# Kernel optimization log

Hardware: AMD Instinct MI355X
Metric: run time of the kernel (lower is better)

Reference implementation:

```python
import jax, jax.numpy as jnp
import numpy as np

B, S, D, V, H, L, NM = 16, 512, 768, 30522, 12, 12, 77
HD = D // H  # 64
FF = 4 * D
EPS = 1e-5


def setup_inputs() -> dict:
    key = jax.random.key(0)
    ks = jax.random.split(key, 32)
    sc = 0.02
    n = lambda k, shp: jax.random.normal(k, shp, dtype=jnp.float32) * sc
    d = {}
    d["token_ids"] = jax.random.randint(ks[0], (B, S), 0, V)
    d["segment_ids"] = jax.random.randint(ks[1], (B, S), 0, 2)
    d["mask_ids"] = jax.random.randint(ks[2], (B, NM), 0, S)
    d["tok_emb"] = n(ks[3], (V, D))
    d["pos_emb"] = n(ks[4], (S, D))
    d["seg_emb"] = n(ks[5], (2, D))
    d["dense_w"] = n(ks[6], (V, D))
    d["dense_b"] = jnp.zeros((V,), jnp.float32)
    # per-layer params stacked on leading L axis (torch Linear convention: y = x @ W.T + b)
    d["Wq"] = n(ks[7], (L, D, D)); d["bq"] = jnp.zeros((L, D), jnp.float32)
    d["Wk"] = n(ks[8], (L, D, D)); d["bk"] = jnp.zeros((L, D), jnp.float32)
    d["Wv"] = n(ks[9], (L, D, D)); d["bv"] = jnp.zeros((L, D), jnp.float32)
    d["Wo"] = n(ks[10], (L, D, D)); d["bo"] = jnp.zeros((L, D), jnp.float32)
    d["W1"] = n(ks[11], (L, FF, D)); d["b1"] = jnp.zeros((L, FF), jnp.float32)
    d["W2"] = n(ks[12], (L, D, FF)); d["b2"] = jnp.zeros((L, D), jnp.float32)
    d["g1"] = jnp.ones((L, D), jnp.float32); d["be1"] = jnp.zeros((L, D), jnp.float32)
    d["g2"] = jnp.ones((L, D), jnp.float32); d["be2"] = jnp.zeros((L, D), jnp.float32)
    return d


def _ln(x, g, b):
    m = jnp.mean(x, -1, keepdims=True)
    v = jnp.mean(jnp.square(x - m), -1, keepdims=True)
    return (x - m) * jax.lax.rsqrt(v + EPS) * g + b


def _encoder_stack(x, layer_params):
    def layer(x, p):
        Wq, bq, Wk, bk, Wv, bv, Wo, bo, W1, b1, W2, b2, g1, be1, g2, be2 = p
        q = (x @ Wq.T + bq).reshape(B, S, H, HD).transpose(0, 2, 1, 3)  # bhsd
        k = (x @ Wk.T + bk).reshape(B, S, H, HD).transpose(0, 2, 1, 3)
        v = (x @ Wv.T + bv).reshape(B, S, H, HD).transpose(0, 2, 1, 3)
        scores = jnp.einsum('bhqd,bhkd->bhqk', q, k) / jnp.sqrt(jnp.float32(HD))
        attn = jax.nn.softmax(scores, axis=-1)
        o = jnp.einsum('bhqk,bhkd->bhqd', attn, v).transpose(0, 2, 1, 3).reshape(B, S, D)
        x = _ln(x + (o @ Wo.T + bo), g1, be1)
        h = jax.nn.gelu(x @ W1.T + b1, approximate=False)  # torch nn.GELU default is exact
        h = h @ W2.T + b2
        return _ln(x + h, g2, be2), None
    x, _ = jax.lax.scan(layer, x, layer_params)
    return x


def reference(token_ids, segment_ids, mask_ids, tok_emb, pos_emb, seg_emb,
              dense_w, dense_b, Wq, bq, Wk, bk, Wv, bv, Wo, bo,
              W1, b1, W2, b2, g1, be1, g2, be2):
    x = tok_emb[token_ids] + seg_emb[segment_ids] + pos_emb[None, :, :]  # [B,S,D]
    x = _encoder_stack(x, (Wq, bq, Wk, bk, Wv, bv, Wo, bo, W1, b1, W2, b2, g1, be1, g2, be2))
    idx = jnp.broadcast_to(mask_ids[:, :, None], (B, NM, D))
    out = jnp.take_along_axis(x, idx, axis=1)  # [B,NM,D]
    return out @ dense_w.T + dense_b  # [B,NM,V]
```

## Files before the change

kernel.cpp:

```cpp
#include <hip/hip_runtime.h>
#include <stdint.h>

typedef uint16_t u16;
typedef uint32_t u32;
typedef uint64_t u64;
typedef short short8 __attribute__((ext_vector_type(8)));
typedef float f32x4 __attribute__((ext_vector_type(4)));

#define DEV static __device__ __forceinline__

DEV u16 f2bf(float f){
  u32 x = __builtin_bit_cast(u32, f);
  return (u16)((x + 0x7fffu + ((x >> 16) & 1u)) >> 16);
}

DEV f32x4 mfma16(short8 a, short8 b, f32x4 c){
  return __builtin_amdgcn_mfma_f32_16x16x32_bf16(a, b, c, 0, 0, 0);
}

DEV void async16(const void* g, void* l){
  __builtin_amdgcn_global_load_lds(
      (const __attribute__((address_space(1))) u32*)g,
      (__attribute__((address_space(3))) u32*)l, 16, 0, 0);
}

__global__ __launch_bounds__(256)
void embed_kernel(const int* __restrict__ tid, const int* __restrict__ sid,
                  const float* __restrict__ tok, const float* __restrict__ pos,
                  const float* __restrict__ seg,
                  float* __restrict__ x, u16* __restrict__ xb)
{
  const int row = blockIdx.x;
  const int s = row & 511;
  const int tk = tid[row], sg = sid[row];
  const int t = threadIdx.x;
#pragma unroll
  for (int e = 0; e < 3; ++e){
    int i = t + e*256;
    float v = tok[(u64)tk*768 + i] + seg[(u64)sg*768 + i] + pos[(u64)s*768 + i];
    x[(u64)row*768 + i] = v;
    xb[(u64)row*768 + i] = f2bf(v);
  }
}

__global__ __launch_bounds__(256)
void cvt_bf16(const float4* __restrict__ in, ushort4* __restrict__ out, int n4)
{
  int i = blockIdx.x*256 + threadIdx.x;
  if (i >= n4) return;
  float4 f = in[i];
  ushort4 o;
  o.x = f2bf(f.x); o.y = f2bf(f.y); o.z = f2bf(f.z); o.w = f2bf(f.w);
  out[i] = o;
}

__global__ __launch_bounds__(256)
void cvt_layer(const float4* __restrict__ Wq, const float4* __restrict__ Wk,
               const float4* __restrict__ Wv, const float4* __restrict__ Wo,
               const float4* __restrict__ W1, const float4* __restrict__ W2,
               ushort4* __restrict__ wqkv, ushort4* __restrict__ wob,
               ushort4* __restrict__ w1b, ushort4* __restrict__ w2b)
{
  const int i = blockIdx.x*256 + threadIdx.x;
  const int S = 147456;
  float4 f; ushort4* dst; int di;
  if      (i <   S)       { f = Wq[i];            dst = wqkv; di = i; }
  else if (i < 2*S)       { f = Wk[i - S];        dst = wqkv; di = i; }
  else if (i < 3*S)       { f = Wv[i - 2*S];      dst = wqkv; di = i; }
  else if (i < 4*S)       { f = Wo[i - 3*S];      dst = wob;  di = i - 3*S; }
  else if (i < 4*S+589824){ f = W1[i - 4*S];      dst = w1b;  di = i - 4*S; }
  else                    { f = W2[i - 4*S-589824]; dst = w2b; di = i - 4*S - 589824; }
  ushort4 o;
  o.x = f2bf(f.x); o.y = f2bf(f.y); o.z = f2bf(f.z); o.w = f2bf(f.w);
  dst[di] = o;
}

__global__ __launch_bounds__(256)
void concat_bias(const float* __restrict__ bq, const float* __restrict__ bk,
                 const float* __restrict__ bv, float* __restrict__ out)
{
  const int l = blockIdx.x;
  const int t = threadIdx.x;
#pragma unroll
  for (int e = 0; e < 3; ++e){
    int i = t + e*256;
    out[(u64)l*2304 + i]        = bq[(u64)l*768 + i];
    out[(u64)l*2304 + 768 + i]  = bk[(u64)l*768 + i];
    out[(u64)l*2304 + 1536 + i] = bv[(u64)l*768 + i];
  }
}

template<int EPI>
__global__ __launch_bounds__(256)
void gemm_db(const u16* __restrict__ A, const u16* __restrict__ W,
             const float* __restrict__ bias, void* __restrict__ Cout,
             int M, int N, int K, int GM)
{
  __shared__ u16 smbuf[16384];
  u16* As = smbuf;
  u16* Ws = smbuf + 8192;
  const int t = threadIdx.x;
  const int w = t >> 6, l = t & 63;
  const int lr = l & 15, lg = l >> 4;

  const int nwg = gridDim.x;
  const int orig = blockIdx.x;
  const int q = nwg >> 3, r = nwg & 7;
  const int xcd = orig & 7, slot = orig >> 3;
  const int wgid = (xcd < r ? xcd*(q+1) : r*(q+1) + (xcd-r)*q) + slot;
  const int bm = wgid % GM, bn = wgid / GM;

  const u16* srcp[4];
  u16* ldsp[4];
#pragma unroll
  for (int i = 0; i < 4; ++i){
    int c = w*4 + i;
    int rt = (c & 7)*16 + (l >> 2);
    int col = (l & 3)*8;
    if (c < 8){
      int row = bm*128 + rt; if (row > M-1) row = M-1;
      srcp[i] = A + (u64)row*K + col;
      ldsp[i] = &As[c*512 + l*8];
    } else {
      int row = bn*128 + rt; if (row > N-1) row = N-1;
      srcp[i] = W + (u64)row*K + col;
      ldsp[i] = &Ws[(c - 8)*512 + l*8];
    }
  }

  const int wm = (w >> 1)*64, wn = (w & 1)*64;
  f32x4 acc[4][4] = {};

  const int nt = K >> 5;
  int buf = 0;
#pragma unroll
  for (int i = 0; i < 4; ++i) async16(srcp[i], ldsp[i]);
  __syncthreads();

  for (int kt = 0; kt < nt; ++kt){
    if (kt + 1 < nt){
      const int k0 = (kt + 1) << 5;
#pragma unroll
      for (int i = 0; i < 4; ++i) async16(srcp[i] + k0, ldsp[i] + (buf ^ 1)*4096);
    }
    short8 af[4], wf[4];
#pragma unroll
    for (int mi = 0; mi < 4; ++mi)
      af[mi] = *(const short8*)(&As[buf*4096 + (wm + mi*16 + lr)*32 + lg*8]);
#pragma unroll
    for (int ni = 0; ni < 4; ++ni)
      wf[ni] = *(const short8*)(&Ws[buf*4096 + (wn + ni*16 + lr)*32 + lg*8]);
#pragma unroll
    for (int mi = 0; mi < 4; ++mi)
#pragma unroll
      for (int ni = 0; ni < 4; ++ni)
        acc[mi][ni] = mfma16(af[mi], wf[ni], acc[mi][ni]);
    if (kt + 1 < nt){
      __syncthreads();
      buf ^= 1;
    }
  }

  __syncthreads();
  constexpr int EPLD = 68;
  float* epw = (float*)smbuf + w*(16*EPLD);
#pragma unroll
  for (int mi = 0; mi < 4; ++mi){
#pragma unroll
    for (int ni = 0; ni < 4; ++ni){
      int col = bn*128 + wn + ni*16 + lr;
      float bv = bias ? bias[col < N ? col : N-1] : 0.f;
#pragma unroll
      for (int rr = 0; rr < 4; ++rr){
        float v = acc[mi][ni][rr] + bv;
        if constexpr (EPI == 2) v = 0.5f*v*(1.0f + erff(v*0.70710678118f));
        epw[(lg*4 + rr)*EPLD + ni*16 + lr] = v;
      }
    }
    asm volatile("s_waitcnt lgkmcnt(0)" ::: "memory");
    if constexpr (EPI == 0){
#pragma unroll
      for (int ps = 0; ps < 4; ++ps){
        int rloc = ps*4 + (l >> 4);
        int row = bm*128 + wm + mi*16 + rloc;
        int col = bn*128 + wn + (l & 15)*4;
        f32x4 v4 = *(const f32x4*)&epw[rloc*EPLD + (l & 15)*4];
        if (row < M){
          if (col + 3 < N) *(f32x4*)((float*)Cout + (u64)row*N + col) = v4;
          else {
#pragma unroll
            for (int j = 0; j < 4; ++j)
              if (col + j < N) ((float*)Cout)[(u64)row*N + col + j] = v4[j];
          }
        }
      }
    } else {
#pragma unroll
      for (int ps = 0; ps < 2; ++ps){
        int rloc = ps*8 + (l >> 3);
        int row = bm*128 + wm + mi*16 + rloc;
        int col = bn*128 + wn + (l & 7)*8;
        f32x4 a4 = *(const f32x4*)&epw[rloc*EPLD + (l & 7)*8];
        f32x4 b4 = *(const f32x4*)&epw[rloc*EPLD + (l & 7)*8 + 4];
        short8 o8;
        o8[0] = f2bf(a4[0]); o8[1] = f2bf(a4[1]); o8[2] = f2bf(a4[2]); o8[3] = f2bf(a4[3]);
        o8[4] = f2bf(b4[0]); o8[5] = f2bf(b4[1]); o8[6] = f2bf(b4[2]); o8[7] = f2bf(b4[3]);
        if (row < M){
          if (col + 7 < N) *(short8*)((u16*)Cout + (u64)row*N + col) = o8;
          else {
#pragma unroll
            for (int j = 0; j < 8; ++j)
              if (col + j < N) ((u16*)Cout)[(u64)row*N + col + j] = (u16)o8[j];
          }
        }
      }
    }
    asm volatile("s_waitcnt lgkmcnt(0)" ::: "memory");
  }
}

DEV void stage_tile(const u16* __restrict__ X, int ld, int limit,
                    int rowbase, int k0, u16* lds, int t)
{
  const int rl  = t >> 2;
  const int col = (((t & 3) ^ ((t >> 3) & 3))) << 3;
  int r0 = rowbase + rl;        if (r0 > limit-1) r0 = limit-1;
  int r1 = rowbase + rl + 128;  if (r1 > limit-1) r1 = limit-1;
  async16(X + (u64)r0*ld + k0 + col, lds + t*8);
  async16(X + (u64)r1*ld + k0 + col, lds + 4096 + t*8);
}

DEV short8 ldfrag(const u16* buf, int row, int slot){
  return *(const short8*)(buf + row*32 + (slot << 3));
}

template<int EPI>
__global__ __launch_bounds__(512)
void gemm8(const u16* __restrict__ A, const u16* __restrict__ W,
           const float* __restrict__ bias, void* __restrict__ Cout,
           int M, int N, int Ksp, int lda, int ldw, int GM, int nsplit,
           u64 cstride)
{
  __shared__ u16 sm[49152];
  u16* Ab = sm;
  u16* Bb = sm + 24576;
  const int t = threadIdx.x;
  const int w = t >> 6, l = t & 63;
  const int lr = l & 15, lg = l >> 4;
  const int wr = w >> 2, wc = w & 3;
  const int xr = (lr >> 1) & 3;
  const int slot = lg ^ xr;

  const int nwg = gridDim.x, orig = blockIdx.x;
  const int q = nwg >> 3, r = nwg & 7;
  const int xcd = orig & 7, sl8 = orig >> 3;
  const int wgid = (xcd < r ? xcd*(q+1) : r*(q+1) + (xcd-r)*q) + sl8;
  const int per = nwg / nsplit;
  const int split = wgid / per;
  const int rem = wgid % per;
  const int bm = rem % GM, bn = rem / GM;
  const int koff = split * Ksp;

  f32x4 acc[8][4] = {};
  short8 afr[4], bfr[4];

  const int NT = Ksp >> 5;
  stage_tile(A, lda, M, bm*256, koff,      Ab,        t);
  stage_tile(W, ldw, N, bn*256, koff,      Bb,        t);
  if (NT > 1){
    stage_tile(A, lda, M, bm*256, koff + 32, Ab + 8192, t);
    stage_tile(W, ldw, N, bn*256, koff + 32, Bb + 8192, t);
  }
  asm volatile("s_waitcnt vmcnt(4)" ::: "memory");
  __builtin_amdgcn_s_barrier();

  for (int tt = 0; tt < NT; ++tt){
    const int rs = (tt % 3) * 8192;
    const int rs2 = ((tt + 2) % 3) * 8192;
    const int k2 = koff + (tt + 2)*32;
    const u16* Ar = Ab + rs;
    const u16* Br = Bb + rs;
#pragma unroll
    for (int mi = 0; mi < 4; ++mi) afr[mi] = ldfrag(Ar, wr*128 + mi*16 + lr, slot);
#pragma unroll
    for (int ni = 0; ni < 4; ++ni) bfr[ni] = ldfrag(Br, wc*64 + ni*16 + lr, slot);
    if (tt + 2 < NT) stage_tile(A, lda, M, bm*256, k2, Ab + rs2, t);
    __builtin_amdgcn_s_barrier();
    __builtin_amdgcn_s_setprio(1);
#pragma unroll
    for (int mi = 0; mi < 4; ++mi)
#pragma unroll
      for (int ni = 0; ni < 4; ++ni)
        acc[mi][ni] = mfma16(afr[mi], bfr[ni], acc[mi][ni]);
    __builtin_amdgcn_s_setprio(0);
    __builtin_amdgcn_s_barrier();
#pragma unroll
    for (int mi = 0; mi < 4; ++mi) afr[mi] = ldfrag(Ar, wr*128 + (mi+4)*16 + lr, slot);
    if (tt + 2 < NT) stage_tile(W, ldw, N, bn*256, k2, Bb + rs2, t);
    __builtin_amdgcn_s_barrier();
    __builtin_amdgcn_s_setprio(1);
#pragma unroll
    for (int mi = 0; mi < 4; ++mi)
#pragma unroll
      for (int ni = 0; ni < 4; ++ni)
        acc[mi+4][ni] = mfma16(afr[mi], bfr[ni], acc[mi+4][ni]);
    __builtin_amdgcn_s_setprio(0);
    if (tt + 2 < NT) asm volatile("s_waitcnt vmcnt(4)" ::: "memory");
    else             asm volatile("s_waitcnt vmcnt(0)" ::: "memory");
    __builtin_amdgcn_s_barrier();
  }

  __syncthreads();
  constexpr int EPLD = 68;
  float* epw = (float*)sm + w*(16*EPLD);
  const int growbase = bm*256 + wr*128;
  const int gcolbase = bn*256 + wc*64;
#pragma unroll
  for (int mi = 0; mi < 8; ++mi){
#pragma unroll
    for (int ni = 0; ni < 4; ++ni){
      int col = gcolbase + ni*16 + lr;
      float bv = (bias && split == 0) ? bias[col < N ? col : N-1] : 0.f;
#pragma unroll
      for (int rr = 0; rr < 4; ++rr){
        float v = acc[mi][ni][rr] + bv;
        if constexpr (EPI == 2) v = 0.5f*v*(1.0f + erff(v*0.70710678118f));
        epw[(lg*4 + rr)*EPLD + ni*16 + lr] = v;
      }
    }
    asm volatile("s_waitcnt lgkmcnt(0)" ::: "memory");
    if constexpr (EPI == 0){
      float* outp = (float*)Cout + (u64)split*cstride;
#pragma unroll
      for (int ps = 0; ps < 4; ++ps){
        int rloc = ps*4 + (l >> 4);
        int row = growbase + mi*16 + rloc;
        int col = gcolbase + (l & 15)*4;
        f32x4 v4 = *(const f32x4*)&epw[rloc*EPLD + (l & 15)*4];
        if (row < M){
          if (col + 3 < N) *(f32x4*)(outp + (u64)row*N + col) = v4;
          else {
#pragma unroll
            for (int j = 0; j < 4; ++j)
              if (col + j < N) outp[(u64)row*N + col + j] = v4[j];
          }
        }
      }
    } else {
#pragma unroll
      for (int ps = 0; ps < 2; ++ps){
        int rloc = ps*8 + (l >> 3);
        int row = growbase + mi*16 + rloc;
        int col = gcolbase + (l & 7)*8;
        f32x4 a4 = *(const f32x4*)&epw[rloc*EPLD + (l & 7)*8];
        f32x4 b4 = *(const f32x4*)&epw[rloc*EPLD + (l & 7)*8 + 4];
        short8 o8;
        o8[0] = f2bf(a4[0]); o8[1] = f2bf(a4[1]); o8[2] = f2bf(a4[2]); o8[3] = f2bf(a4[3]);
        o8[4] = f2bf(b4[0]); o8[5] = f2bf(b4[1]); o8[6] = f2bf(b4[2]); o8[7] = f2bf(b4[3]);
        if (row < M){
          if (col + 7 < N) *(short8*)((u16*)Cout + (u64)row*N + col) = o8;
          else {
#pragma unroll
            for (int j = 0; j < 8; ++j)
              if (col + j < N) ((u16*)Cout)[(u64)row*N + col + j] = (u16)o8[j];
          }
        }
      }
    }
    asm volatile("s_waitcnt lgkmcnt(0)" ::: "memory");
  }
}

__global__ __launch_bounds__(256)
void transpose_v(const u16* __restrict__ qkv, u16* __restrict__ vt)
{
  __shared__ u16 tile[64][72];
  const int st = blockIdx.x, h = blockIdx.y, b = blockIdx.z;
  const int t = threadIdx.x;
#pragma unroll
  for (int e = 0; e < 2; ++e){
    int lin = t + e*256;
    int s = lin >> 3, c8 = (lin & 7)*8;
    *(short8*)(&tile[s][c8]) =
        *(const short8*)(qkv + (u64)(b*512 + st*64 + s)*2304 + 1536 + h*64 + c8);
  }
  __syncthreads();
#pragma unroll
  for (int e = 0; e < 2; ++e){
    int lin = t + e*256;
    int d = lin >> 3, s8 = (lin & 7)*8;
    short8 ov;
#pragma unroll
    for (int i = 0; i < 8; ++i) ov[i] = (short)tile[s8 + i][d];
    *(short8*)(vt + ((u64)(b*12 + h)*64 + d)*512 + st*64 + s8) = ov;
  }
}

__global__ __launch_bounds__(256)
void attn_kernel(const u16* __restrict__ qkv, const u16* __restrict__ vt,
                 u16* __restrict__ ob)
{
  __shared__ u16 p_lds[4][16][72];
  const int t = threadIdx.x, w = t >> 6, ll = t & 63;
  const int lr = ll & 15, lg = ll >> 4;
  const int qt = blockIdx.x, h = blockIdx.y, b = blockIdx.z;
  const int q0 = qt*64 + w*16;

  const u16* qrow = qkv + (u64)(b*512 + q0 + lr)*2304 + h*64 + 8*lg;
  const short8 qf0 = *(const short8*)qrow;
  const short8 qf1 = *(const short8*)(qrow + 32);

  const u16* kbh = qkv + (u64)(b*512)*2304 + 768 + h*64;
  const u16* vth = vt + (u64)(b*12 + h)*64*512;

  float m_r[4], l_r[4];
  f32x4 o_acc[4] = {};
#pragma unroll
  for (int r = 0; r < 4; ++r){ m_r[r] = -1e30f; l_r[r] = 0.f; }

  for (int jt = 0; jt < 8; ++jt){
    const int jb = jt*64;
    f32x4 s[4] = {};
#pragma unroll
    for (int jn = 0; jn < 4; ++jn){
      const u16* kr = kbh + (u64)(jb + jn*16 + lr)*2304 + 8*lg;
      short8 kf0 = *(const short8*)kr;
      short8 kf1 = *(const short8*)(kr + 32);
      s[jn] = mfma16(qf0, kf0, s[jn]);
      s[jn] = mfma16(qf1, kf1, s[jn]);
    }
#pragma unroll
    for (int jn = 0; jn < 4; ++jn)
#pragma unroll
      for (int r = 0; r < 4; ++r) s[jn][r] *= 0.125f;

    float mn[4], corr[4], rs[4];
#pragma unroll
    for (int r = 0; r < 4; ++r){
      float v = fmaxf(fmaxf(s[0][r], s[1][r]), fmaxf(s[2][r], s[3][r]));
#pragma unroll
      for (int m = 1; m < 16; m <<= 1) v = fmaxf(v, __shfl_xor(v, m));
      mn[r] = fmaxf(m_r[r], v);
      corr[r] = __expf(m_r[r] - mn[r]);
      m_r[r] = mn[r];
      rs[r] = 0.f;
    }
#pragma unroll
    for (int jn = 0; jn < 4; ++jn)
#pragma unroll
      for (int r = 0; r < 4; ++r){
        float pv = __expf(s[jn][r] - mn[r]);
        s[jn][r] = pv;
        rs[r] += pv;
      }
#pragma unroll
    for (int r = 0; r < 4; ++r){
      float v = rs[r];
#pragma unroll
      for (int m = 1; m < 16; m <<= 1) v += __shfl_xor(v, m);
      l_r[r] = l_r[r]*corr[r] + v;
    }
#pragma unroll
    for (int nd = 0; nd < 4; ++nd)
#pragma unroll
      for (int r = 0; r < 4; ++r) o_acc[nd][r] *= corr[r];

#pragma unroll
    for (int jn = 0; jn < 4; ++jn)
#pragma unroll
      for (int r = 0; r < 4; ++r)
        p_lds[w][4*lg + r][jn*16 + lr] = f2bf(s[jn][r]);
    asm volatile("s_waitcnt lgkmcnt(0)" ::: "memory");
    short8 pa0 = *(const short8*)(&p_lds[w][lr][8*lg]);
    short8 pa1 = *(const short8*)(&p_lds[w][lr][32 + 8*lg]);
#pragma unroll
    for (int nd = 0; nd < 4; ++nd){
      const u16* vr = vth + (u64)(nd*16 + lr)*512 + jb + 8*lg;
      short8 vf0 = *(const short8*)vr;
      short8 vf1 = *(const short8*)(vr + 32);
      o_acc[nd] = mfma16(pa0, vf0, o_acc[nd]);
      o_acc[nd] = mfma16(pa1, vf1, o_acc[nd]);
    }
    asm volatile("s_waitcnt lgkmcnt(0)" ::: "memory");
  }
#pragma unroll
  for (int r = 0; r < 4; ++r) l_r[r] = 1.f / l_r[r];
#pragma unroll
  for (int nd = 0; nd < 4; ++nd)
#pragma unroll
    for (int r = 0; r < 4; ++r)
      p_lds[w][4*lg + r][nd*16 + lr] = f2bf(o_acc[nd][r]*l_r[r]);
  asm volatile("s_waitcnt lgkmcnt(0)" ::: "memory");
#pragma unroll
  for (int ps = 0; ps < 2; ++ps){
    int row = ps*8 + (ll >> 3);
    short8 ov = *(const short8*)(&p_lds[w][row][(ll & 7)*8]);
    *(short8*)(ob + (u64)(b*512 + q0 + row)*768 + h*64 + (ll & 7)*8) = ov;
  }
}

__global__ __launch_bounds__(256)
void ln_res(const float* xin, const float* __restrict__ yin,
            const float* __restrict__ g, const float* __restrict__ be,
            float* xout, u16* __restrict__ xbout)
{
  __shared__ float sred[8];
  const int row = blockIdx.x, t = threadIdx.x;
  const int w = t >> 6, ll = t & 63;
  float v[3]; float s = 0.f, sq = 0.f;
#pragma unroll
  for (int e = 0; e < 3; ++e){
    int i = t + e*256;
    float val = xin[(u64)row*768 + i] + yin[(u64)row*768 + i];
    v[e] = val; s += val; sq += val*val;
  }
#pragma unroll
  for (int m = 1; m < 64; m <<= 1){ s += __shfl_xor(s, m); sq += __shfl_xor(sq, m); }
  if (ll == 0){ sred[w] = s; sred[4 + w] = sq; }
  __syncthreads();
  s  = sred[0] + sred[1] + sred[2] + sred[3];
  sq = sred[4] + sred[5] + sred[6] + sred[7];
  const float mean = s*(1.f/768.f);
  const float rstd = rsqrtf(sq*(1.f/768.f) - mean*mean + 1e-5f);
#pragma unroll
  for (int e = 0; e < 3; ++e){
    int i = t + e*256;
    float o = (v[e] - mean)*rstd*g[i] + be[i];
    xout[(u64)row*768 + i] = o;
    xbout[(u64)row*768 + i] = f2bf(o);
  }
}

__global__ __launch_bounds__(256)
void gather_rows(const u16* __restrict__ xb, const int* __restrict__ mids,
                 u16* __restrict__ xg)
{
  const int row = blockIdx.x;
  const int b = row / 77;
  const int src = b*512 + mids[row];
  const int t = threadIdx.x;
#pragma unroll
  for (int e = 0; e < 3; ++e){
    int i = t + e*256;
    xg[(u64)row*768 + i] = xb[(u64)src*768 + i];
  }
}

extern "C" void kernel_launch(void* const* d_in, const int* in_sizes, int n_in,
                              void* d_out, int out_size, void* d_ws, size_t ws_size,
                              hipStream_t stream)
{
  const int*   token_ids  = (const int*)  d_in[0];
  const int*   segment_ids= (const int*)  d_in[1];
  const int*   mask_ids   = (const int*)  d_in[2];
  const float* tok_emb    = (const float*)d_in[3];
  const float* pos_emb    = (const float*)d_in[4];
  const float* seg_emb    = (const float*)d_in[5];
  const float* dense_w    = (const float*)d_in[6];
  const float* dense_b    = (const float*)d_in[7];
  const float* Wq = (const float*)d_in[8];  const float* bq = (const float*)d_in[9];
  const float* Wk = (const float*)d_in[10]; const float* bk = (const float*)d_in[11];
  const float* Wv = (const float*)d_in[12]; const float* bv = (const float*)d_in[13];
  const float* Wo = (const float*)d_in[14]; const float* bo = (const float*)d_in[15];
  const float* W1 = (const float*)d_in[16]; const float* b1 = (const float*)d_in[17];
  const float* W2 = (const float*)d_in[18]; const float* b2 = (const float*)d_in[19];
  const float* g1 = (const float*)d_in[20]; const float* be1= (const float*)d_in[21];
  const float* g2 = (const float*)d_in[22]; const float* be2= (const float*)d_in[23];

  char* p = (char*)d_ws;
  auto alloc = [&](size_t bytes)->char*{
    char* r = p; p += (bytes + 255) & ~(size_t)255; return r;
  };
  const u64 T = 8192;
  float* x    = (float*)alloc(T*768*4);
  float* y    = (float*)alloc(T*768*4);
  u16*   xb   = (u16*)  alloc(T*768*2);
  u16*   qkvb = (u16*)  alloc(T*2304*2);
  u16*   vT   = (u16*)  alloc(T*768*2);
  u16*   obuf = (u16*)  alloc(T*768*2);
  u16*   h1b  = (u16*)  alloc(T*3072*2);
  u16*   xg   = (u16*)  alloc((u64)1232*768*2);
  u16*   wqkv = (u16*)  alloc((u64)2304*768*2);
  u16*   wob  = (u16*)  alloc((u64)768*768*2);
  u16*   w1b  = (u16*)  alloc((u64)3072*768*2);
  u16*   w2b  = (u16*)  alloc((u64)3072*768*2);
  float* bqkv = (float*)alloc((u64)12*2304*4);
  u16*   dwb  = h1b;

  if ((size_t)(p - (char*)d_ws) > ws_size) return;

  embed_kernel<<<dim3(8192), dim3(256), 0, stream>>>(
      token_ids, segment_ids, tok_emb, pos_emb, seg_emb, x, xb);
  concat_bias<<<dim3(12), dim3(256), 0, stream>>>(bq, bk, bv, bqkv);

  for (int l = 0; l < 12; ++l){
    cvt_layer<<<dim3(6912), dim3(256), 0, stream>>>(
        (const float4*)(Wq + (u64)l*589824), (const float4*)(Wk + (u64)l*589824),
        (const float4*)(Wv + (u64)l*589824), (const float4*)(Wo + (u64)l*589824),
        (const float4*)(W1 + (u64)l*2359296), (const float4*)(W2 + (u64)l*2359296),
        (ushort4*)wqkv, (ushort4*)wob, (ushort4*)w1b, (ushort4*)w2b);

    gemm_db<1><<<dim3(18*64), dim3(256), 0, stream>>>(xb, wqkv, bqkv + (u64)l*2304, qkvb, 8192, 2304, 768, 64);

    transpose_v<<<dim3(8, 12, 16), dim3(256), 0, stream>>>(qkvb, vT);
    attn_kernel<<<dim3(8, 12, 16), dim3(256), 0, stream>>>(qkvb, vT, obuf);

    gemm_db<0><<<dim3(6*64), dim3(256), 0, stream>>>(obuf, wob, bo + (u64)l*768, y, 8192, 768, 768, 64);
    ln_res<<<dim3(8192), dim3(256), 0, stream>>>(x, y, g1 + (u64)l*768, be1 + (u64)l*768, x, xb);

    gemm_db<2><<<dim3(24*64), dim3(256), 0, stream>>>(xb, w1b, b1 + (u64)l*3072, h1b, 8192, 3072, 768, 64);
    gemm_db<0><<<dim3(6*64), dim3(256), 0, stream>>>(h1b, w2b, b2 + (u64)l*768, y, 8192, 768, 3072, 64);
    ln_res<<<dim3(8192), dim3(256), 0, stream>>>(x, y, g2 + (u64)l*768, be2 + (u64)l*768, x, xb);
  }

  gather_rows<<<dim3(1232), dim3(256), 0, stream>>>(xb, mask_ids, xg);
  cvt_bf16<<<dim3(22892), dim3(256), 0, stream>>>((const float4*)dense_w, (ushort4*)dwb, 5860224);
  gemm8<0><<<dim3(5*120), dim3(512), 0, stream>>>(xg, dwb, dense_b, (float*)d_out,
                                                  1232, 30522, 768, 768, 768, 5, 1, 0);
}
```

Before: 4.318 ms.

## Replace double-buffered encoder GEMM with triple-buffered, split-phase pipelined kernel

Replaces the encoder GEMM with a version that keeps three LDS stages, so loads for the tile two steps ahead are issued while the current tile is computed. Each K step is split into two halves, each with its own loads and a raised wave priority around the MFMA burst. Tiles are stored with XOR-swizzled column slots to reduce LDS bank conflicts. The goal is to hide global-load latency and cut stalls on the synchronisation barrier. In exchange it uses more LDS per block, which may reduce occupancy, and the barrier and vmcnt logic is more fragile.

```diff
diff --git a/kernel.cpp b/kernel.cpp
--- a/kernel.cpp
+++ b/kernel.cpp
@@ -90,80 +90,94 @@
   }
 }
 
+DEV void stage128(const u16* __restrict__ X, int ld, int limit,
+                  int rowbase, int k0, u16* lds, int t)
+{
+  const int rl  = t >> 2;
+  const int col = (((t & 3) ^ ((t >> 3) & 3))) << 3;
+  int r0 = rowbase + rl;       if (r0 > limit-1) r0 = limit-1;
+  int r1 = rowbase + rl + 64;  if (r1 > limit-1) r1 = limit-1;
+  async16(X + (u64)r0*ld + k0 + col, lds + t*8);
+  async16(X + (u64)r1*ld + k0 + col, lds + 2048 + t*8);
+}
+
+DEV short8 ldfrag(const u16* buf, int row, int slot){
+  return *(const short8*)(buf + row*32 + (slot << 3));
+}
+
 template<int EPI>
 __global__ __launch_bounds__(256)
-void gemm_db(const u16* __restrict__ A, const u16* __restrict__ W,
-             const float* __restrict__ bias, void* __restrict__ Cout,
-             int M, int N, int K, int GM)
-{
-  __shared__ u16 smbuf[16384];
-  u16* As = smbuf;
-  u16* Ws = smbuf + 8192;
+void gemm3r(const u16* __restrict__ A, const u16* __restrict__ W,
+            const float* __restrict__ bias, void* __restrict__ Cout,
+            int M, int N, int K, int GM)
+{
+  __shared__ u16 sm[24576];
   const int t = threadIdx.x;
   const int w = t >> 6, l = t & 63;
   const int lr = l & 15, lg = l >> 4;
-
-  const int nwg = gridDim.x;
-  const int orig = blockIdx.x;
+  const int wm = (w >> 1)*64, wn = (w & 1)*64;
+  const int xr = (lr >> 1) & 3;
+  const int slot = lg ^ xr;
+
+  const int nwg = gridDim.x, orig = blockIdx.x;
   const int q = nwg >> 3, r = nwg & 7;
-  const int xcd = orig & 7, slot = orig >> 3;
-  const int wgid = (xcd < r ? xcd*(q+1) : r*(q+1) + (xcd-r)*q) + slot;
+  const int xcd = orig & 7, sl8 = orig >> 3;
+  const int wgid = (xcd < r ? xcd*(q+1) : r*(q+1) + (xcd-r)*q) + sl8;
   const int bm = wgid % GM, bn = wgid / GM;
 
-  const u16* srcp[4];
-  u16* ldsp[4];
-#pragma unroll
-  for (int i = 0; i < 4; ++i){
-    int c = w*4 + i;
-    int rt = (c & 7)*16 + (l >> 2);
-    int col = (l & 3)*8;
-    if (c < 8){
-      int row = bm*128 + rt; if (row > M-1) row = M-1;
-      srcp[i] = A + (u64)row*K + col;
-      ldsp[i] = &As[c*512 + l*8];
-    } else {
-      int row = bn*128 + rt; if (row > N-1) row = N-1;
-      srcp[i] = W + (u64)row*K + col;
-      ldsp[i] = &Ws[(c - 8)*512 + l*8];
-    }
-  }
-
-  const int wm = (w >> 1)*64, wn = (w & 1)*64;
   f32x4 acc[4][4] = {};
-
-  const int nt = K >> 5;
-  int buf = 0;
-#pragma unroll
-  for (int i = 0; i < 4; ++i) async16(srcp[i], ldsp[i]);
-  __syncthreads();
-
-  for (int kt = 0; kt < nt; ++kt){
-    if (kt + 1 < nt){
-      const int k0 = (kt + 1) << 5;
-#pragma unroll
-      for (int i = 0; i < 4; ++i) async16(srcp[i] + k0, ldsp[i] + (buf ^ 1)*4096);
-    }
-    short8 af[4], wf[4];
-#pragma unroll
-    for (int mi = 0; mi < 4; ++mi)
-      af[mi] = *(const short8*)(&As[buf*4096 + (wm + mi*16 + lr)*32 + lg*8]);
-#pragma unroll
-    for (int ni = 0; ni < 4; ++ni)
-      wf[ni] = *(const short8*)(&Ws[buf*4096 + (wn + ni*16 + lr)*32 + lg*8]);
-#pragma unroll
-    for (int mi = 0; mi < 4; ++mi)
+  short8 af[4], bf[4];
+
+  const int NT = K >> 5;
+  stage128(A, K, M, bm*128,  0, sm,          t);
+  stage128(W, K, N, bn*128,  0, sm + 4096,   t);
+  stage128(A, K, M, bm*128, 32, sm + 8192,   t);
+  stage128(W, K, N, bn*128, 32, sm + 12288,  t);
+  asm volatile("s_waitcnt vmcnt(4)" ::: "memory");
+  __builtin_amdgcn_s_barrier();
+
+  for (int tt = 0; tt < NT; ++tt){
+    const int rs  = (tt % 3) * 8192;
+    const int rs2 = ((tt + 2) % 3) * 8192;
+    const int k2  = (tt + 2) * 32;
+    const bool st2 = (tt + 2) < NT;
+    const u16* Ar = sm + rs;
+    const u16* Br = sm + rs + 4096;
+
+    af[0] = ldfrag(Ar, wm + lr, slot);
+    af[1] = ldfrag(Ar, wm + 16 + lr, slot);
+#pragma unroll
+    for (int ni = 0; ni < 4; ++ni) bf[ni] = ldfrag(Br, wn + ni*16 + lr, slot);
+    if (st2) stage128(A, K, M, bm*128, k2, sm + rs2, t);
+    __builtin_amdgcn_s_barrier();
+    __builtin_amdgcn_s_setprio(1);
+#pragma unroll
+    for (int mi = 0; mi < 2; ++mi)
 #pragma unroll
       for (int ni = 0; ni < 4; ++ni)
-        acc[mi][ni] = mfma16(af[mi], wf[ni], acc[mi][ni]);
-    if (kt + 1 < nt){
-      __syncthreads();
-      buf ^= 1;
-    }
+        acc[mi][ni] = mfma16(af[mi], bf[ni], acc[mi][ni]);
+    __builtin_amdgcn_s_setprio(0);
+    __builtin_amdgcn_s_barrier();
+
+    af[2] = ldfrag(Ar, wm + 32 + lr, slot);
+    af[3] = ldfrag(Ar, wm + 48 + lr, slot);
+    if (st2) stage128(W, K, N, bn*128, k2, sm + rs2 + 4096, t);
+    __builtin_amdgcn_s_barrier();
+    __builtin_amdgcn_s_setprio(1);
+#pragma unroll
+    for (int mi = 2; mi < 4; ++mi)
+#pragma unroll
+      for (int ni = 0; ni < 4; ++ni)
+        acc[mi][ni] = mfma16(af[mi], bf[ni], acc[mi][ni]);
+    __builtin_amdgcn_s_setprio(0);
+    if (st2) asm volatile("s_waitcnt vmcnt(4)" ::: "memory");
+    else     asm volatile("s_waitcnt vmcnt(0)" ::: "memory");
+    __builtin_amdgcn_s_barrier();
   }
 
   __syncthreads();
   constexpr int EPLD = 68;
-  float* epw = (float*)smbuf + w*(16*EPLD);
+  float* epw = (float*)sm + w*(16*EPLD);
 #pragma unroll
   for (int mi = 0; mi < 4; ++mi){
 #pragma unroll
@@ -228,10 +242,6 @@
   int r1 = rowbase + rl + 128;  if (r1 > limit-1) r1 = limit-1;
   async16(X + (u64)r0*ld + k0 + col, lds + t*8);
   async16(X + (u64)r1*ld + k0 + col, lds + 4096 + t*8);
-}
-
-DEV short8 ldfrag(const u16* buf, int row, int slot){
-  return *(const short8*)(buf + row*32 + (slot << 3));
 }
 
 template<int EPI>
@@ -600,16 +610,20 @@
         (const float4*)(W1 + (u64)l*2359296), (const float4*)(W2 + (u64)l*2359296),
         (ushort4*)wqkv, (ushort4*)wob, (ushort4*)w1b, (ushort4*)w2b);
 
-    gemm_db<1><<<dim3(18*64), dim3(256), 0, stream>>>(xb, wqkv, bqkv + (u64)l*2304, qkvb, 8192, 2304, 768, 64);
+    gemm3r<1><<<dim3(64*18), dim3(256), 0, stream>>>(xb, wqkv, bqkv + (u64)l*2304, qkvb,
+                                                     8192, 2304, 768, 64);
 
     transpose_v<<<dim3(8, 12, 16), dim3(256), 0, stream>>>(qkvb, vT);
     attn_kernel<<<dim3(8, 12, 16), dim3(256), 0, stream>>>(qkvb, vT, obuf);
 
-    gemm_db<0><<<dim3(6*64), dim3(256), 0, stream>>>(obuf, wob, bo + (u64)l*768, y, 8192, 768, 768, 64);
+    gemm3r<0><<<dim3(64*6), dim3(256), 0, stream>>>(obuf, wob, bo + (u64)l*768, y,
+                                                    8192, 768, 768, 64);
     ln_res<<<dim3(8192), dim3(256), 0, stream>>>(x, y, g1 + (u64)l*768, be1 + (u64)l*768, x, xb);
 
-    gemm_db<2><<<dim3(24*64), dim3(256), 0, stream>>>(xb, w1b, b1 + (u64)l*3072, h1b, 8192, 3072, 768, 64);
-    gemm_db<0><<<dim3(6*64), dim3(256), 0, stream>>>(h1b, w2b, b2 + (u64)l*768, y, 8192, 768, 3072, 64);
+    gemm3r<2><<<dim3(64*24), dim3(256), 0, stream>>>(xb, w1b, b1 + (u64)l*3072, h1b,
+                                                     8192, 3072, 768, 64);
+    gemm3r<0><<<dim3(64*6), dim3(256), 0, stream>>>(h1b, w2b, b2 + (u64)l*768, y,
+                                                    8192, 768, 3072, 64);
     ln_res<<<dim3(8192), dim3(256), 0, stream>>>(x, y, g2 + (u64)l*768, be2 + (u64)l*768, x, xb);
   }
 
```

After: 4.221 ms. 2.3% less time.
